# Performance work log

Measured on AMD Instinct MI355X. Metric: run time of the kernel, lower is better.

## Reference

```python
import jax, jax.numpy as jnp
import numpy as np

N_NODES = 100000
N_EDGES = 1200000
F_IN = 128
HIDDEN = 64
N_CLASSES = 2


def gcn_layer(h_in, W, b, src_sl, dst_sl, norm, n):
    # GCNConv: X' = D^{-1/2} (A + I) D^{-1/2} X W + b
    h = h_in @ W                              # [N, F_out] dense projection
    msg = h[src_sl] * norm[:, None]           # gather + per-edge normalization
    return jax.ops.segment_sum(msg, dst_sl, num_segments=n) + b  # scatter-add


def _prep_edges(edge_index, n, dtype):
    # add self-loops (PyG GCNConv default) and compute symmetric norm
    loops = jnp.arange(n, dtype=edge_index.dtype)
    src_sl = jnp.concatenate([edge_index[0], loops])
    dst_sl = jnp.concatenate([edge_index[1], loops])
    deg = jax.ops.segment_sum(jnp.ones_like(dst_sl, dtype=dtype), dst_sl, num_segments=n)
    d_inv_sqrt = jnp.where(deg > 0, jax.lax.rsqrt(deg), 0.0).astype(dtype)
    norm = d_inv_sqrt[src_sl] * d_inv_sqrt[dst_sl]
    return src_sl, dst_sl, norm


def setup_inputs() -> dict:
    key = jax.random.key(0)
    k1, k2, k3, k4 = jax.random.split(key, 4)
    x = jax.random.normal(k1, (N_NODES, F_IN), dtype=jnp.float32)
    edge_index = jax.random.randint(k2, (2, N_EDGES), 0, N_NODES, dtype=jnp.int64)
    # glorot-scaled weights like PyG GCNConv defaults
    W1 = jax.random.normal(k3, (F_IN, HIDDEN), dtype=jnp.float32) * (1.0 / np.sqrt(F_IN))
    b1 = jnp.zeros((HIDDEN,), dtype=jnp.float32)
    W2 = jax.random.normal(k4, (HIDDEN, N_CLASSES), dtype=jnp.float32) * (1.0 / np.sqrt(HIDDEN))
    b2 = jnp.zeros((N_CLASSES,), dtype=jnp.float32)
    return {"x": x, "W1": W1, "b1": b1, "W2": W2, "b2": b2, "edge_index": edge_index}


def reference(x, W1, b1, W2, b2, edge_index):
    n = x.shape[0]
    src_sl, dst_sl, norm = _prep_edges(edge_index, n, x.dtype)
    h = jax.nn.relu(gcn_layer(x, W1, b1, src_sl, dst_sl, norm, n))
    out = gcn_layer(h, W2, b2, src_sl, dst_sl, norm, n)
    return jax.nn.log_softmax(out, axis=1)
```

## Files before the change

### kernel.cpp

```cpp
#include <hip/hip_runtime.h>
#include <math.h>

#define N_NODES 100000
#define N_EDGES 1200000
#define F_IN 128
#define HIDDEN 64
#define CAP 40
#define RB 64
#define XS_STRIDE 136
#define NRANGE 8
#define FILL_CHUNKS 256
#define FILL_BLOCKS (NRANGE * FILL_CHUNKS)

typedef unsigned short u16;
struct __align__(8) U16x4 { u16 x, y, z, w; };

__device__ __forceinline__ u16 f2bf(float f) {
    unsigned int u = __float_as_uint(f);
    return (u16)((u + 0x7fffu + ((u >> 16) & 1u)) >> 16);
}
__device__ __forceinline__ float bf2f(u16 h) {
    return __uint_as_float((unsigned int)h << 16);
}


__global__ void zero_kernel(int* __restrict__ cnt, int n) {
    int i = blockIdx.x * blockDim.x + threadIdx.x;
    if (i < n) cnt[i] = 0;
}


__global__ __launch_bounds__(256) void fill_kernel(const int* __restrict__ src,
                                                   const int* __restrict__ dst,
                                                   int* __restrict__ cnt,
                                                   int* __restrict__ csr) {
    const int range = blockIdx.x & (NRANGE - 1);
    const int chunk = blockIdx.x >> 3;
    const int lo = range * (N_NODES / NRANGE);
    const int hi = lo + (N_NODES / NRANGE);
    const int QUADS = N_EDGES / 4;
    const int perq = (QUADS + FILL_CHUNKS - 1) / FILL_CHUNKS;
    int q0 = chunk * perq;
    int q1 = q0 + perq; if (q1 > QUADS) q1 = QUADS;
    for (int q = q0 + threadIdx.x; q < q1; q += 256) {
        int4 d4 = ((const int4*)dst)[q];
        int4 s4 = ((const int4*)src)[q];
#pragma unroll
        for (int j = 0; j < 4; ++j) {
            int d = (j == 0) ? d4.x : (j == 1) ? d4.y : (j == 2) ? d4.z : d4.w;
            if (d >= lo && d < hi) {
                int s = (j == 0) ? s4.x : (j == 1) ? s4.y : (j == 2) ? s4.z : s4.w;
                int p = atomicAdd(&cnt[d], 1);
                if (p < CAP) csr[(size_t)d * CAP + p] = s;
            }
        }
    }
}


__global__ __launch_bounds__(256) void gemm1_kernel(const float* __restrict__ x,
                                                    const float* __restrict__ W1,
                                                    const int* __restrict__ cnt,
                                                    u16* __restrict__ hn16) {
    __shared__ float w[F_IN * HIDDEN];
    __shared__ u16 xs[RB * XS_STRIDE];
    const int tid = threadIdx.x;
    const int row0 = blockIdx.x * RB;
    {
        const float4* wg = (const float4*)W1;
        float4* wl = (float4*)w;
        for (int i = tid; i < F_IN * HIDDEN / 4; i += 256) wl[i] = wg[i];
        for (int i = tid; i < RB * F_IN / 4; i += 256) {
            int r = i / (F_IN / 4), c4 = (i % (F_IN / 4)) * 4;
            int gr = row0 + r;
            float4 v = {0.f, 0.f, 0.f, 0.f};
            if (gr < N_NODES) v = *(const float4*)&x[(size_t)gr * F_IN + c4];
            U16x4 b = {f2bf(v.x), f2bf(v.y), f2bf(v.z), f2bf(v.w)};
            *(U16x4*)&xs[r * XS_STRIDE + c4] = b;
        }
    }
    __syncthreads();
    const int tx = tid & 15;
    const int ty = tid >> 4;
    const int c = tx * 4;
    float acc[4][4] = {{0.f}};
#pragma unroll 4
    for (int kp = 0; kp < F_IN; kp += 2) {
        const float4 w0 = *(const float4*)&w[kp * HIDDEN + c];
        const float4 w1 = *(const float4*)&w[(kp + 1) * HIDDEN + c];
#pragma unroll
        for (int rr = 0; rr < 4; ++rr) {
            unsigned int u = *(const unsigned int*)&xs[(ty * 4 + rr) * XS_STRIDE + kp];
            float xlo = __uint_as_float(u << 16);
            float xhi = __uint_as_float(u & 0xffff0000u);
            acc[rr][0] = fmaf(xhi, w1.x, fmaf(xlo, w0.x, acc[rr][0]));
            acc[rr][1] = fmaf(xhi, w1.y, fmaf(xlo, w0.y, acc[rr][1]));
            acc[rr][2] = fmaf(xhi, w1.z, fmaf(xlo, w0.z, acc[rr][2]));
            acc[rr][3] = fmaf(xhi, w1.w, fmaf(xlo, w0.w, acc[rr][3]));
        }
    }
#pragma unroll
    for (int rr = 0; rr < 4; ++rr) {
        int row = row0 + ty * 4 + rr;
        if (row < N_NODES) {
            float dd = rsqrtf((float)(cnt[row] + 1));
            U16x4 o = {f2bf(acc[rr][0] * dd), f2bf(acc[rr][1] * dd),
                       f2bf(acc[rr][2] * dd), f2bf(acc[rr][3] * dd)};
            *(U16x4*)&hn16[(size_t)row * HIDDEN + c] = o;
        }
    }
}


__global__ __launch_bounds__(256) void gather1_kernel(const u16* __restrict__ hn16,
                                                      const int* __restrict__ cnt,
                                                      const int* __restrict__ csr,
                                                      const float* __restrict__ b1,
                                                      const float* __restrict__ W2,
                                                      float* __restrict__ h2n) {
    int v = (blockIdx.x * 256 + threadIdx.x) >> 6;
    int lane = threadIdx.x & 63;
    if (v >= N_NODES) return;
    int deg = cnt[v];
    float dd = rsqrtf((float)(deg + 1));
    int n = deg > CAP ? CAP : deg;
    const int* idx = csr + (size_t)v * CAP;
    float acc = 0.f;
    int i = 0;
    for (; i + 8 <= n; i += 8) {
        int4 q0 = *(const int4*)&idx[i];
        int4 q1 = *(const int4*)&idx[i + 4];
        float a0 = bf2f(hn16[(size_t)q0.x * HIDDEN + lane]);
        float a1 = bf2f(hn16[(size_t)q0.y * HIDDEN + lane]);
        float a2 = bf2f(hn16[(size_t)q0.z * HIDDEN + lane]);
        float a3 = bf2f(hn16[(size_t)q0.w * HIDDEN + lane]);
        float a4 = bf2f(hn16[(size_t)q1.x * HIDDEN + lane]);
        float a5 = bf2f(hn16[(size_t)q1.y * HIDDEN + lane]);
        float a6 = bf2f(hn16[(size_t)q1.z * HIDDEN + lane]);
        float a7 = bf2f(hn16[(size_t)q1.w * HIDDEN + lane]);
        acc += ((a0 + a1) + (a2 + a3)) + ((a4 + a5) + (a6 + a7));
    }
    if (i + 4 <= n) {
        int4 q = *(const int4*)&idx[i];
        float a0 = bf2f(hn16[(size_t)q.x * HIDDEN + lane]);
        float a1 = bf2f(hn16[(size_t)q.y * HIDDEN + lane]);
        float a2 = bf2f(hn16[(size_t)q.z * HIDDEN + lane]);
        float a3 = bf2f(hn16[(size_t)q.w * HIDDEN + lane]);
        acc += (a0 + a1) + (a2 + a3);
        i += 4;
    }
    for (; i < n; ++i) {
        acc += bf2f(hn16[(size_t)idx[i] * HIDDEN + lane]);
    }
    float val = dd * (acc + bf2f(hn16[(size_t)v * HIDDEN + lane])) + b1[lane];
    val = fmaxf(val, 0.f);
    float2 wv = *(const float2*)&W2[lane * 2];
    float s0 = val * wv.x;
    float s1 = val * wv.y;
#pragma unroll
    for (int m = 32; m >= 1; m >>= 1) {
        s0 += __shfl_xor(s0, m, 64);
        s1 += __shfl_xor(s1, m, 64);
    }
    if (lane == 0) {
        float2 o = {dd * s0, dd * s1};
        *(float2*)&h2n[(size_t)v * 2] = o;
    }
}


__global__ void gather2_kernel(const float* __restrict__ h2n, const int* __restrict__ cnt,
                               const int* __restrict__ csr, const float* __restrict__ b2,
                               float* __restrict__ out) {
    int v = blockIdx.x * blockDim.x + threadIdx.x;
    if (v >= N_NODES) return;
    int deg = cnt[v];
    float dd = rsqrtf((float)(deg + 1));
    int n = deg > CAP ? CAP : deg;
    const int* idx = csr + (size_t)v * CAP;
    float a0 = 0.f, a1 = 0.f;
    int i = 0;
    for (; i + 8 <= n; i += 8) {
        int4 q0 = *(const int4*)&idx[i];
        int4 q1 = *(const int4*)&idx[i + 4];
        float2 h0 = *(const float2*)&h2n[(size_t)q0.x * 2];
        float2 h1 = *(const float2*)&h2n[(size_t)q0.y * 2];
        float2 h2 = *(const float2*)&h2n[(size_t)q0.z * 2];
        float2 h3 = *(const float2*)&h2n[(size_t)q0.w * 2];
        float2 h4 = *(const float2*)&h2n[(size_t)q1.x * 2];
        float2 h5 = *(const float2*)&h2n[(size_t)q1.y * 2];
        float2 h6 = *(const float2*)&h2n[(size_t)q1.z * 2];
        float2 h7 = *(const float2*)&h2n[(size_t)q1.w * 2];
        a0 += ((h0.x + h1.x) + (h2.x + h3.x)) + ((h4.x + h5.x) + (h6.x + h7.x));
        a1 += ((h0.y + h1.y) + (h2.y + h3.y)) + ((h4.y + h5.y) + (h6.y + h7.y));
    }
    if (i + 4 <= n) {
        int4 q = *(const int4*)&idx[i];
        float2 h0 = *(const float2*)&h2n[(size_t)q.x * 2];
        float2 h1 = *(const float2*)&h2n[(size_t)q.y * 2];
        float2 h2 = *(const float2*)&h2n[(size_t)q.z * 2];
        float2 h3 = *(const float2*)&h2n[(size_t)q.w * 2];
        a0 += (h0.x + h1.x) + (h2.x + h3.x);
        a1 += (h0.y + h1.y) + (h2.y + h3.y);
        i += 4;
    }
    for (; i < n; ++i) {
        float2 hv = *(const float2*)&h2n[(size_t)idx[i] * 2];
        a0 += hv.x; a1 += hv.y;
    }
    float2 hs = *(const float2*)&h2n[(size_t)v * 2];
    float v0 = dd * (a0 + hs.x) + b2[0];
    float v1 = dd * (a1 + hs.y) + b2[1];
    float m = fmaxf(v0, v1);
    float ls = m + logf(__expf(v0 - m) + __expf(v1 - m));
    float2 o = {v0 - ls, v1 - ls};
    *(float2*)&out[(size_t)v * 2] = o;
}


extern "C" void kernel_launch(void* const* d_in, const int* in_sizes, int n_in,
                              void* d_out, int out_size, void* d_ws, size_t ws_size,
                              hipStream_t stream) {
    const float* x  = (const float*)d_in[0];
    const float* W1 = (const float*)d_in[1];
    const float* b1 = (const float*)d_in[2];
    const float* W2 = (const float*)d_in[3];
    const float* b2 = (const float*)d_in[4];
    const int* edge_index = (const int*)d_in[5];
    const int* src = edge_index;
    const int* dst = edge_index + N_EDGES;
    float* out = (float*)d_out;

    char* ws = (char*)d_ws;
    size_t off = 0;
    auto alloc = [&](size_t bytes) {
        void* p = ws + off;
        off = (off + bytes + 255) & ~(size_t)255;
        return p;
    };
    int*   cnt  = (int*)alloc(N_NODES * sizeof(int));
    int*   csr  = (int*)alloc((size_t)N_NODES * CAP * sizeof(int));
    u16*   hn16 = (u16*)alloc((size_t)N_NODES * HIDDEN * sizeof(u16));
    float* h2n  = (float*)alloc((size_t)N_NODES * 2 * sizeof(float));
    (void)ws_size;

    const int B = 256;
    const int NB_N = (N_NODES + B - 1) / B;

    zero_kernel<<<NB_N, B, 0, stream>>>(cnt, N_NODES);
    fill_kernel<<<FILL_BLOCKS, B, 0, stream>>>(src, dst, cnt, csr);

    gemm1_kernel<<<(N_NODES + RB - 1) / RB, B, 0, stream>>>(x, W1, cnt, hn16);

    gather1_kernel<<<N_NODES * 64 / B, B, 0, stream>>>(hn16, cnt, csr, b1, W2, h2n);

    gather2_kernel<<<NB_N, B, 0, stream>>>(h2n, cnt, csr, b2, out);
}
```

Measured before the change: 236.9 us.

## Use bf16 MFMA instructions for the first-layer projection GEMM

Replaces the scalar FMA tiled GEMM for x@W1 with MFMA 16x16x32 bf16 instructions. Each wave loads its A fragments straight from global memory into registers, and W1 is stored transposed as bf16 in shared memory. This removes the staging of x through shared memory and the scalar FMA work. The output stores become 2-byte scattered writes per lane instead of 8-byte vector stores, which may cost some write efficiency.

Result: faster. 220.3 us (-7.0%).

```diff
diff --git a/kernel.cpp b/kernel.cpp
--- a/kernel.cpp
+++ b/kernel.cpp
@@ -6,14 +6,15 @@
 #define F_IN 128
 #define HIDDEN 64
 #define CAP 40
-#define RB 64
-#define XS_STRIDE 136
 #define NRANGE 8
 #define FILL_CHUNKS 256
 #define FILL_BLOCKS (NRANGE * FILL_CHUNKS)
+#define GROWS 64
+#define WT_STRIDE 136
 
 typedef unsigned short u16;
-struct __align__(8) U16x4 { u16 x, y, z, w; };
+typedef __attribute__((ext_vector_type(8))) short short8v;
+typedef __attribute__((ext_vector_type(4))) float float4v;
 
 __device__ __forceinline__ u16 f2bf(float f) {
     unsigned int u = __float_as_uint(f);
@@ -62,51 +63,57 @@
                                                     const float* __restrict__ W1,
                                                     const int* __restrict__ cnt,
                                                     u16* __restrict__ hn16) {
-    __shared__ float w[F_IN * HIDDEN];
-    __shared__ u16 xs[RB * XS_STRIDE];
+    __shared__ u16 wt[HIDDEN * WT_STRIDE];
     const int tid = threadIdx.x;
-    const int row0 = blockIdx.x * RB;
-    {
-        const float4* wg = (const float4*)W1;
-        float4* wl = (float4*)w;
-        for (int i = tid; i < F_IN * HIDDEN / 4; i += 256) wl[i] = wg[i];
-        for (int i = tid; i < RB * F_IN / 4; i += 256) {
-            int r = i / (F_IN / 4), c4 = (i % (F_IN / 4)) * 4;
-            int gr = row0 + r;
-            float4 v = {0.f, 0.f, 0.f, 0.f};
-            if (gr < N_NODES) v = *(const float4*)&x[(size_t)gr * F_IN + c4];
-            U16x4 b = {f2bf(v.x), f2bf(v.y), f2bf(v.z), f2bf(v.w)};
-            *(U16x4*)&xs[r * XS_STRIDE + c4] = b;
+    for (int i = tid; i < F_IN * HIDDEN; i += 256) {
+        int k = i >> 6, c = i & 63;
+        wt[c * WT_STRIDE + k] = f2bf(W1[i]);
+    }
+    __syncthreads();
+
+    const int wave = tid >> 6, lane = tid & 63;
+    const int rbase = blockIdx.x * GROWS + wave * 16;
+    const int arow = rbase + (lane & 15);
+    const int arl = arow < N_NODES ? arow : N_NODES - 1;
+    const int kslice = (lane >> 4) * 8;
+
+    short8v a[4];
+#pragma unroll
+    for (int ks = 0; ks < 4; ++ks) {
+        const float* xp = &x[(size_t)arl * F_IN + ks * 32 + kslice];
+        float4 v0 = *(const float4*)xp;
+        float4 v1 = *(const float4*)(xp + 4);
+        short8v av;
+        av[0] = (short)f2bf(v0.x); av[1] = (short)f2bf(v0.y);
+        av[2] = (short)f2bf(v0.z); av[3] = (short)f2bf(v0.w);
+        av[4] = (short)f2bf(v1.x); av[5] = (short)f2bf(v1.y);
+        av[6] = (short)f2bf(v1.z); av[7] = (short)f2bf(v1.w);
+        a[ks] = av;
+    }
+
+    float dd[4];
+    int crow[4];
+#pragma unroll
+    for (int r = 0; r < 4; ++r) {
+        crow[r] = rbase + (lane >> 4) * 4 + r;
+        int rc = crow[r] < N_NODES ? crow[r] : N_NODES - 1;
+        dd[r] = rsqrtf((float)(cnt[rc] + 1));
+    }
+
+    const int colb = lane & 15;
+#pragma unroll
+    for (int ct = 0; ct < 4; ++ct) {
+        float4v acc = {0.f, 0.f, 0.f, 0.f};
+#pragma unroll
+        for (int ks = 0; ks < 4; ++ks) {
+            short8v b = *(const short8v*)&wt[(ct * 16 + colb) * WT_STRIDE + ks * 32 + kslice];
+            acc = __builtin_amdgcn_mfma_f32_16x16x32_bf16(a[ks], b, acc, 0, 0, 0);
         }
-    }
-    __syncthreads();
-    const int tx = tid & 15;
-    const int ty = tid >> 4;
-    const int c = tx * 4;
-    float acc[4][4] = {{0.f}};
-#pragma unroll 4
-    for (int kp = 0; kp < F_IN; kp += 2) {
-        const float4 w0 = *(const float4*)&w[kp * HIDDEN + c];
-        const float4 w1 = *(const float4*)&w[(kp + 1) * HIDDEN + c];
-#pragma unroll
-        for (int rr = 0; rr < 4; ++rr) {
-            unsigned int u = *(const unsigned int*)&xs[(ty * 4 + rr) * XS_STRIDE + kp];
-            float xlo = __uint_as_float(u << 16);
-            float xhi = __uint_as_float(u & 0xffff0000u);
-            acc[rr][0] = fmaf(xhi, w1.x, fmaf(xlo, w0.x, acc[rr][0]));
-            acc[rr][1] = fmaf(xhi, w1.y, fmaf(xlo, w0.y, acc[rr][1]));
-            acc[rr][2] = fmaf(xhi, w1.z, fmaf(xlo, w0.z, acc[rr][2]));
-            acc[rr][3] = fmaf(xhi, w1.w, fmaf(xlo, w0.w, acc[rr][3]));
-        }
-    }
-#pragma unroll
-    for (int rr = 0; rr < 4; ++rr) {
-        int row = row0 + ty * 4 + rr;
-        if (row < N_NODES) {
-            float dd = rsqrtf((float)(cnt[row] + 1));
-            U16x4 o = {f2bf(acc[rr][0] * dd), f2bf(acc[rr][1] * dd),
-                       f2bf(acc[rr][2] * dd), f2bf(acc[rr][3] * dd)};
-            *(U16x4*)&hn16[(size_t)row * HIDDEN + c] = o;
+#pragma unroll
+        for (int r = 0; r < 4; ++r) {
+            if (crow[r] < N_NODES) {
+                hn16[(size_t)crow[r] * HIDDEN + ct * 16 + colb] = f2bf(acc[r] * dd[r]);
+            }
         }
     }
 }
@@ -250,7 +257,7 @@
     zero_kernel<<<NB_N, B, 0, stream>>>(cnt, N_NODES);
     fill_kernel<<<FILL_BLOCKS, B, 0, stream>>>(src, dst, cnt, csr);
 
-    gemm1_kernel<<<(N_NODES + RB - 1) / RB, B, 0, stream>>>(x, W1, cnt, hn16);
+    gemm1_kernel<<<(N_NODES + GROWS - 1) / GROWS, B, 0, stream>>>(x, W1, cnt, hn16);
 
     gather1_kernel<<<N_NODES * 64 / B, B, 0, stream>>>(hn16, cnt, csr, b1, W2, h2n);
 
```
